# Kernel tuning notes

Hardware: AMD Instinct MI355X
Metric: run time of the kernel (lower is better)

The kernel has to match this reference:

```python
import jax, jax.numpy as jnp
import numpy as np

D_IN = 1024
D_OUT = 1024
NUM_HEADS = 16
HEAD_DIM = D_OUT // NUM_HEADS


def setup_inputs() -> dict:
    key = jax.random.key(0)
    k_x, k_qkv, k_pw, k_pb = jax.random.split(key, 4)
    x = jax.random.normal(k_x, (2, 2048, D_IN), dtype=jnp.float32)
    # torch nn.Linear(d_in, 3*d_out, bias=False): weight [3*d_out, d_in]
    w_qkv = jax.random.normal(k_qkv, (3 * D_OUT, D_IN), dtype=jnp.float32) * (1.0 / np.sqrt(D_IN))
    # proj: nn.Linear(d_out, d_out) with bias
    w_proj = jax.random.normal(k_pw, (D_OUT, D_OUT), dtype=jnp.float32) * (1.0 / np.sqrt(D_OUT))
    b_proj = jax.random.normal(k_pb, (D_OUT,), dtype=jnp.float32) * 0.01
    return {"x": x, "w_qkv": w_qkv, "w_proj": w_proj, "b_proj": b_proj}


def reference(x, w_qkv, w_proj, b_proj):
    B, S, _ = x.shape
    # fused QKV projection: [B,S,3*D_OUT]
    qkv = jnp.einsum('bsd,ed->bse', x, w_qkv)
    qkv = qkv.reshape(B, S, 3, NUM_HEADS, HEAD_DIM)
    q, k, v = jnp.moveaxis(qkv, 2, 0)  # each [B,S,H,Dh]
    scale = 1.0 / jnp.sqrt(jnp.asarray(HEAD_DIM, dtype=x.dtype))
    # scores [B,H,S,S]
    scores = jnp.einsum('bqhd,bkhd->bhqk', q, k) * scale
    causal = jnp.tril(jnp.ones((S, S), dtype=bool))
    scores = jnp.where(causal, scores, jnp.asarray(-jnp.inf, dtype=scores.dtype))
    attn = jax.nn.softmax(scores, axis=-1)
    ctx = jnp.einsum('bhqk,bkhd->bqhd', attn, v)  # [B,S,H,Dh]
    ctx = ctx.reshape(B, S, D_OUT)
    return jnp.einsum('bsd,ed->bse', ctx, w_proj) + b_proj
```

## Files before the change

kernel.cpp:

```cpp
#include <hip/hip_runtime.h>
#include <hip/hip_bf16.h>
#include <cstdint>

#define B_SZ   2
#define S_LEN  2048
#define NH     16
#define NT     32
#define LDA    72

using f32x4 = __attribute__((ext_vector_type(4))) float;
typedef __bf16 bf16x8 __attribute__((ext_vector_type(8)));
typedef __bf16 bf16x4 __attribute__((ext_vector_type(4)));

__device__ inline float bf2f(unsigned short u) {
    union { unsigned int i; float f; } v; v.i = ((unsigned int)u) << 16; return v.f;
}
__device__ inline unsigned short f2bf(float f) {
    union { float f; unsigned int i; } v; v.f = f;
    unsigned int r = v.i + 0x7fff + ((v.i >> 16) & 1);
    return (unsigned short)(r >> 16);
}
__device__ inline f32x4 mfma16(bf16x8 a, bf16x8 b, f32x4 c) {
    return __builtin_amdgcn_mfma_f32_16x16x32_bf16(a, b, c, 0, 0, 0);
}
__device__ inline void stC(float* C, size_t idx, float v)  { C[idx] = v; }
__device__ inline void stC(__bf16* C, size_t idx, float v) { ((unsigned short*)C)[idx] = f2bf(v); }

__global__ __launch_bounds__(256) void f2b2_kernel(
    const float* __restrict__ a, int na4, __bf16* __restrict__ outa,
    const float* __restrict__ b, int nb4, __bf16* __restrict__ outb)
{
    int i = blockIdx.x * blockDim.x + threadIdx.x;
    const float* src; __bf16* dst; int idx;
    if (i < na4)           { src = a; dst = outa; idx = i; }
    else if (i < na4 + nb4){ src = b; dst = outb; idx = i - na4; }
    else return;
    float4 v = ((const float4*)src)[idx];
    ushort4 o;
    o.x = f2bf(v.x); o.y = f2bf(v.y); o.z = f2bf(v.z); o.w = f2bf(v.w);
    ((ushort4*)dst)[idx] = o;
}

__global__ __launch_bounds__(256) void f2b_kernel(
    const float* __restrict__ in, __bf16* __restrict__ out, int n4)
{
    int i = blockIdx.x * blockDim.x + threadIdx.x;
    if (i < n4) {
        float4 v = ((const float4*)in)[i];
        ushort4 o;
        o.x = f2bf(v.x); o.y = f2bf(v.y); o.z = f2bf(v.z); o.w = f2bf(v.w);
        ((ushort4*)out)[i] = o;
    }
}

template <typename TO, int HAS_BIAS>
__global__ __launch_bounds__(256) void gemm128(
    const __bf16* __restrict__ A, const __bf16* __restrict__ W,
    const float* __restrict__ bias, TO* __restrict__ C,
    int M, int N, int K)
{
    __shared__ __bf16 Alds[2][128 * 32];
    __shared__ __bf16 Blds[2][128 * 32];
    const int tid  = threadIdx.x, lane = tid & 63, w = tid >> 6;
    const int c16  = lane & 15, quad = lane >> 4;
    const int mBase = blockIdx.y * 128, nBase = blockIdx.x * 128;
    const int moff = (w & 1) * 64, noff = (w >> 1) * 64;

    f32x4 acc[4][4];
#pragma unroll
    for (int i = 0; i < 4; ++i)
#pragma unroll
        for (int j = 0; j < 4; ++j) acc[i][j] = (f32x4){0.f, 0.f, 0.f, 0.f};

    auto stage = [&](int buf, int k0) {
#pragma unroll
        for (int p = 0; p < 2; ++p) {
            const int linear = p * 256 + tid;
            const int row = linear >> 2;
            const int seg = (linear & 3) ^ (row & 3);
            const int lbase = (p * 256 + w * 64) * 8;
            const __bf16* ga = A + (size_t)(mBase + row) * K + k0 + seg * 8;
            const __bf16* gb = W + (size_t)(nBase + row) * K + k0 + seg * 8;
            __builtin_amdgcn_global_load_lds(
                (const __attribute__((address_space(1))) void*)ga,
                (__attribute__((address_space(3))) void*)(&Alds[buf][lbase]), 16, 0, 0);
            __builtin_amdgcn_global_load_lds(
                (const __attribute__((address_space(1))) void*)gb,
                (__attribute__((address_space(3))) void*)(&Blds[buf][lbase]), 16, 0, 0);
        }
    };

    stage(0, 0);
    int cur = 0;
    for (int k0 = 0; k0 < K; k0 += 32) {
        __syncthreads();
        if (k0 + 32 < K) stage(cur ^ 1, k0 + 32);

        bf16x8 af[4], bw[4];
#pragma unroll
        for (int i = 0; i < 4; ++i) {
            const int rowA = moff + i * 16 + c16;
            af[i] = *(const bf16x8*)&Alds[cur][rowA * 32 + ((quad ^ (rowA & 3)) << 3)];
            const int rowB = noff + i * 16 + c16;
            bw[i] = *(const bf16x8*)&Blds[cur][rowB * 32 + ((quad ^ (rowB & 3)) << 3)];
        }
#pragma unroll
        for (int i = 0; i < 4; ++i)
#pragma unroll
            for (int j = 0; j < 4; ++j)
                acc[i][j] = mfma16(af[i], bw[j], acc[i][j]);
        cur ^= 1;
    }

#pragma unroll
    for (int j = 0; j < 4; ++j) {
        const int col = nBase + noff + j * 16 + c16;
        const float bv = HAS_BIAS ? bias[col] : 0.f;
#pragma unroll
        for (int i = 0; i < 4; ++i)
#pragma unroll
            for (int r = 0; r < 4; ++r) {
                const int row = mBase + moff + i * 16 + quad * 4 + r;
                stC(C, (size_t)row * N + col, acc[i][j][r] + bv);
            }
    }
}

template <typename TO, int HAS_BIAS>
__global__ __launch_bounds__(256) void gemm64(
    const __bf16* __restrict__ A, const __bf16* __restrict__ W,
    const float* __restrict__ bias, TO* __restrict__ C,
    int M, int N, int K)
{
    __shared__ __bf16 Alds[2][64 * 32];
    __shared__ __bf16 Blds[2][128 * 32];
    const int tid  = threadIdx.x, lane = tid & 63, w = tid >> 6;
    const int c16  = lane & 15, quad = lane >> 4;
    const int mBase = blockIdx.y * 64, nBase = blockIdx.x * 128;
    const int moff = (w & 1) * 32, noff = (w >> 1) * 64;

    f32x4 acc[2][4];
#pragma unroll
    for (int i = 0; i < 2; ++i)
#pragma unroll
        for (int j = 0; j < 4; ++j) acc[i][j] = (f32x4){0.f, 0.f, 0.f, 0.f};

    auto stage = [&](int buf, int k0) {
        {
            const int row = tid >> 2;
            const int seg = (tid & 3) ^ (row & 3);
            const int lbase = (w * 64) * 8;
            const __bf16* ga = A + (size_t)(mBase + row) * K + k0 + seg * 8;
            __builtin_amdgcn_global_load_lds(
                (const __attribute__((address_space(1))) void*)ga,
                (__attribute__((address_space(3))) void*)(&Alds[buf][lbase]), 16, 0, 0);
        }
#pragma unroll
        for (int p = 0; p < 2; ++p) {
            const int linear = p * 256 + tid;
            const int row = linear >> 2;
            const int seg = (linear & 3) ^ (row & 3);
            const int lbase = (p * 256 + w * 64) * 8;
            const __bf16* gb = W + (size_t)(nBase + row) * K + k0 + seg * 8;
            __builtin_amdgcn_global_load_lds(
                (const __attribute__((address_space(1))) void*)gb,
                (__attribute__((address_space(3))) void*)(&Blds[buf][lbase]), 16, 0, 0);
        }
    };

    stage(0, 0);
    int cur = 0;
    for (int k0 = 0; k0 < K; k0 += 32) {
        __syncthreads();
        if (k0 + 32 < K) stage(cur ^ 1, k0 + 32);

        bf16x8 af[2], bw[4];
#pragma unroll
        for (int i = 0; i < 2; ++i) {
            const int rowA = moff + i * 16 + c16;
            af[i] = *(const bf16x8*)&Alds[cur][rowA * 32 + ((quad ^ (rowA & 3)) << 3)];
        }
#pragma unroll
        for (int j = 0; j < 4; ++j) {
            const int rowB = noff + j * 16 + c16;
            bw[j] = *(const bf16x8*)&Blds[cur][rowB * 32 + ((quad ^ (rowB & 3)) << 3)];
        }
#pragma unroll
        for (int i = 0; i < 2; ++i)
#pragma unroll
            for (int j = 0; j < 4; ++j)
                acc[i][j] = mfma16(af[i], bw[j], acc[i][j]);
        cur ^= 1;
    }

#pragma unroll
    for (int j = 0; j < 4; ++j) {
        const int col = nBase + noff + j * 16 + c16;
        const float bv = HAS_BIAS ? bias[col] : 0.f;
#pragma unroll
        for (int i = 0; i < 2; ++i)
#pragma unroll
            for (int r = 0; r < 4; ++r) {
                const int row = mBase + moff + i * 16 + quad * 4 + r;
                stC(C, (size_t)row * N + col, acc[i][j][r] + bv);
            }
    }
}

__global__ __launch_bounds__(256) void attn(
    const __bf16* __restrict__ qkv, __bf16* __restrict__ ctx,
    float* __restrict__ opart, float* __restrict__ lpart)
{
    __shared__ __bf16 Qs[64 * LDA];
    __shared__ __bf16 Ks[64 * LDA];
    __shared__ __bf16 Vs[64 * LDA];
    __shared__ __bf16 Ps[64 * LDA];

    const int tid  = threadIdx.x;
    const int lane = tid & 63;
    const int w    = tid >> 6;
    const int c16  = lane & 15;
    const int quad = lane >> 4;
    const int bh = blockIdx.x, b = bh >> 4, h = bh & 15;
    const int y  = blockIdx.y;

    int qt, c0, c1, seg;
    bool split;
    if (y < 16)      { qt = 16 + y; const int half = (qt + 2) >> 1; c0 = 0;    c1 = half;   split = true;  seg = 0; }
    else if (y < 32) { qt = y;      const int half = (qt + 2) >> 1; c0 = half; c1 = qt + 1; split = true;  seg = 1; }
    else             { qt = 47 - y; c0 = 0; c1 = qt + 1; split = false; seg = 0; }
    const int qBase = qt * 64;
    const int segIdx = split ? ((bh * 16 + (qt - 16)) * 2 + seg) : 0;

    const float QS = 0.125f * 1.4426950408889634f;

    const int krow0 = tid >> 3;
    const int kd0   = (tid & 7) * 8;
    const int c16t = tid & 15;
    const int jh   = (tid >> 4) & 1;
    const int dblk = tid >> 5;

    const size_t rowB = (size_t)b * S_LEN;
    const __bf16* kp0 = qkv + (rowB + c0 * 64 + krow0) * 3072 + 1024 + h * 64 + kd0;
    const __bf16* kp1 = kp0 + (size_t)32 * 3072;
    const __bf16* vp0 = qkv + (rowB + c0 * 64 + 2 * jh * 16 + c16t) * 3072 + 2048 + h * 64 + dblk * 8;
    const __bf16* vp1 = vp0 + (size_t)16 * 3072;

    uint4 kr0 = *(const uint4*)kp0;
    uint4 kr1 = *(const uint4*)kp1;
    uint4 vr0 = *(const uint4*)vp0;
    uint4 vr1 = *(const uint4*)vp1;

#pragma unroll
    for (int p = 0; p < 2; ++p) {
        const int linear = p * 256 + tid;
        const int row = linear >> 3;
        const int d0 = (linear & 7) * 8;
        const __bf16* g = qkv + (rowB + qBase + row) * 3072 + h * 64 + d0;
        uint4 raw = *(const uint4*)g;
        const unsigned short* u = (const unsigned short*)&raw;
        unsigned short tmp[8];
#pragma unroll
        for (int jj = 0; jj < 8; ++jj) tmp[jj] = f2bf(bf2f(u[jj]) * QS);
        *(uint4*)&Qs[row * LDA + d0] = *(const uint4*)tmp;
    }
    __syncthreads();

    const bf16x8 aq0 = *(const bf16x8*)&Qs[(w * 16 + c16) * LDA + quad * 8];
    const bf16x8 aq1 = *(const bf16x8*)&Qs[(w * 16 + c16) * LDA + 32 + quad * 8];

    float l_r[4] = {0.f, 0.f, 0.f, 0.f};
    f32x4 acc_o[4];
#pragma unroll
    for (int j = 0; j < 4; ++j) acc_o[j] = (f32x4){0.f, 0.f, 0.f, 0.f};

    for (int cc = c0; cc < c1; ++cc) {
        *(uint4*)&Ks[krow0 * LDA + kd0]        = kr0;
        *(uint4*)&Ks[(krow0 + 32) * LDA + kd0] = kr1;
        {
            const unsigned short* e1 = (const unsigned short*)&vr0;
            const unsigned short* e2 = (const unsigned short*)&vr1;
#pragma unroll
            for (int d = 0; d < 8; ++d) {
                const unsigned pack = (unsigned)e1[d] | ((unsigned)e2[d] << 16);
                *(unsigned*)&Vs[(dblk * 8 + d) * LDA + c16t * 4 + 2 * jh] = pack;
            }
        }
        __syncthreads();

        if (cc + 1 < c1) {
            kp0 += (size_t)64 * 3072; kp1 += (size_t)64 * 3072;
            vp0 += (size_t)64 * 3072; vp1 += (size_t)64 * 3072;
            kr0 = *(const uint4*)kp0;
            kr1 = *(const uint4*)kp1;
            vr0 = *(const uint4*)vp0;
            vr1 = *(const uint4*)vp1;
        }

        f32x4 sc[4];
#pragma unroll
        for (int j = 0; j < 4; ++j) sc[j] = (f32x4){0.f, 0.f, 0.f, 0.f};
#pragma unroll
        for (int j = 0; j < 4; ++j) {
            bf16x8 bk0 = *(const bf16x8*)&Ks[(j * 16 + c16) * LDA + quad * 8];
            bf16x8 bk1 = *(const bf16x8*)&Ks[(j * 16 + c16) * LDA + 32 + quad * 8];
            sc[j] = mfma16(aq0, bk0, sc[j]);
            sc[j] = mfma16(aq1, bk1, sc[j]);
        }

        if (cc == qt) {
#pragma unroll
            for (int j = 0; j < 4; ++j) {
                const int key = cc * 64 + j * 16 + c16;
#pragma unroll
                for (int r = 0; r < 4; ++r) {
                    const int q = qBase + w * 16 + quad * 4 + r;
                    if (key > q) sc[j][r] = -1e30f;
                }
            }
        }

        float p_[4][4];
#pragma unroll
        for (int j = 0; j < 4; ++j)
#pragma unroll
            for (int r = 0; r < 4; ++r)
                p_[j][r] = exp2f(sc[j][r]);
#pragma unroll
        for (int r = 0; r < 4; ++r)
            l_r[r] += (p_[0][r] + p_[1][r]) + (p_[2][r] + p_[3][r]);

#pragma unroll
        for (int r = 0; r < 4; ++r) {
            bf16x4 pb;
            pb[0] = (__bf16)p_[0][r]; pb[1] = (__bf16)p_[1][r];
            pb[2] = (__bf16)p_[2][r]; pb[3] = (__bf16)p_[3][r];
            *(bf16x4*)&Ps[(w * 16 + quad * 4 + r) * LDA + c16 * 4] = pb;
        }

        bf16x8 ap0 = *(const bf16x8*)&Ps[(w * 16 + c16) * LDA + quad * 8];
        bf16x8 ap1 = *(const bf16x8*)&Ps[(w * 16 + c16) * LDA + 32 + quad * 8];
#pragma unroll
        for (int j = 0; j < 4; ++j) {
            bf16x8 bv0 = *(const bf16x8*)&Vs[(j * 16 + c16) * LDA + quad * 8];
            bf16x8 bv1 = *(const bf16x8*)&Vs[(j * 16 + c16) * LDA + 32 + quad * 8];
            acc_o[j] = mfma16(ap0, bv0, acc_o[j]);
            acc_o[j] = mfma16(ap1, bv1, acc_o[j]);
        }
        __syncthreads();
    }

    if (!split) {
#pragma unroll
        for (int r = 0; r < 4; ++r) {
            float l = l_r[r];
            l += __shfl_xor(l, 1);
            l += __shfl_xor(l, 2);
            l += __shfl_xor(l, 4);
            l += __shfl_xor(l, 8);
            const float inv = 1.0f / l;
            const size_t rowO = (rowB + qBase + w * 16 + quad * 4 + r) * 1024 + h * 64;
#pragma unroll
            for (int j = 0; j < 4; ++j)
                ctx[rowO + j * 16 + c16] = (__bf16)(acc_o[j][r] * inv);
        }
    } else {
        float* ob = opart + (size_t)segIdx * 4096;
#pragma unroll
        for (int r = 0; r < 4; ++r) {
            float l = l_r[r];
            l += __shfl_xor(l, 1);
            l += __shfl_xor(l, 2);
            l += __shfl_xor(l, 4);
            l += __shfl_xor(l, 8);
            const int qrow = w * 16 + quad * 4 + r;
            if (c16 == 0) lpart[segIdx * 64 + qrow] = l;
#pragma unroll
            for (int j = 0; j < 4; ++j)
                ob[qrow * 64 + j * 16 + c16] = acc_o[j][r];
        }
    }
}

__global__ __launch_bounds__(256) void attn_combine(
    const float* __restrict__ opart, const float* __restrict__ lpart,
    __bf16* __restrict__ ctx)
{
    const int blk = blockIdx.x;
    const int bh = blk >> 4, t = blk & 15;
    const int b = bh >> 4, h = bh & 15;
    const int qt = 16 + t;
    const int tid = threadIdx.x;
    const int q  = tid >> 2;
    const int d0 = (tid & 3) * 16;
    const int segA = blk * 2, segB = segA + 1;
    const float* oa = opart + (size_t)segA * 4096 + q * 64 + d0;
    const float* obp = opart + (size_t)segB * 4096 + q * 64 + d0;
    const float inv = 1.0f / (lpart[segA * 64 + q] + lpart[segB * 64 + q]);
    unsigned short outv[16];
#pragma unroll
    for (int i = 0; i < 4; ++i) {
        float4 a = ((const float4*)oa)[i];
        float4 c = ((const float4*)obp)[i];
        outv[4 * i + 0] = f2bf((a.x + c.x) * inv);
        outv[4 * i + 1] = f2bf((a.y + c.y) * inv);
        outv[4 * i + 2] = f2bf((a.z + c.z) * inv);
        outv[4 * i + 3] = f2bf((a.w + c.w) * inv);
    }
    __bf16* dst = ctx + ((size_t)(b * S_LEN + qt * 64 + q)) * 1024 + h * 64 + d0;
    *(uint4*)dst       = *(const uint4*)&outv[0];
    *(uint4*)(dst + 8) = *(const uint4*)&outv[8];
}

extern "C" void kernel_launch(void* const* d_in, const int* in_sizes, int n_in,
                              void* d_out, int out_size, void* d_ws, size_t ws_size,
                              hipStream_t stream) {
    const float* x      = (const float*)d_in[0];
    const float* w_qkv  = (const float*)d_in[1];
    const float* w_proj = (const float*)d_in[2];
    const float* b_proj = (const float*)d_in[3];
    float* out = (float*)d_out;

    __bf16* qkvb = (__bf16*)d_ws;
    __bf16* xb   = qkvb + (size_t)4096 * 3072;
    __bf16* wqb  = xb + (size_t)4096 * 1024;
    __bf16* ctxb = xb;
    __bf16* wpb  = wqb;
    float*  lpart = (float*)(wqb + (size_t)1024 * 1024);
    float* opart = out;

    const int M = B_SZ * S_LEN;
    const int nx4 = 4096 * 1024 / 4, nq4 = 3072 * 1024 / 4, np4 = 1024 * 1024 / 4;

    f2b2_kernel<<<(nx4 + nq4 + 255) / 256, 256, 0, stream>>>(x, nx4, xb, w_qkv, nq4, wqb);

    gemm128<__bf16, 0><<<dim3(3072 / 128, M / 128), 256, 0, stream>>>(
        xb, wqb, nullptr, qkvb, M, 3072, 1024);

    f2b_kernel<<<(np4 + 255) / 256, 256, 0, stream>>>(w_proj, wpb, np4);

    attn<<<dim3(B_SZ * NH, 48), 256, 0, stream>>>(qkvb, ctxb, opart, lpart);
    attn_combine<<<B_SZ * NH * 16, 256, 0, stream>>>(opart, lpart, ctxb);

    gemm64<float, 1><<<dim3(1024 / 128, M / 64), 256, 0, stream>>>(
        ctxb, wpb, b_proj, out, M, 1024, 1024);
}
```

Before: 184.9 us.

## Enlarge attention query tile to 128 rows with table-driven split scheduling

The attention kernel now processes 128 query rows per block (32 per wave) instead of 64, so each K/V tile loaded into shared memory feeds twice as many MFMAs. Work assignment moves to a constant lookup table that orders tiles largest-first and splits the eight longest query tiles into two key-range segments, with the combine kernel resized to match. This halves the number of blocks and K/V global reloads, at the cost of more registers and shared memory per block, fewer blocks in flight, and a coarser diagonal masking region.

```diff
diff --git a/kernel.cpp b/kernel.cpp
--- a/kernel.cpp
+++ b/kernel.cpp
@@ -5,7 +5,6 @@
 #define B_SZ   2
 #define S_LEN  2048
 #define NH     16
-#define NT     32
 #define LDA    72
 
 using f32x4 = __attribute__((ext_vector_type(4))) float;
@@ -25,6 +24,9 @@
 }
 __device__ inline void stC(float* C, size_t idx, float v)  { C[idx] = v; }
 __device__ inline void stC(__bf16* C, size_t idx, float v) { ((unsigned short*)C)[idx] = f2bf(v); }
+
+__constant__ unsigned char JT[24] = {15,15,7,14,14,13,13,6,12,12,11,11,5,10,10,9,9,4,8,8,3,2,1,0};
+__constant__ unsigned char JM[24] = { 0, 1,2, 0, 1, 0, 1,2, 0, 1, 0, 1,2, 0, 1,0,1,2,0,1,2,2,2,2};
 
 __global__ __launch_bounds__(256) void f2b2_kernel(
     const float* __restrict__ a, int na4, __bf16* __restrict__ outa,
@@ -211,10 +213,10 @@
     const __bf16* __restrict__ qkv, __bf16* __restrict__ ctx,
     float* __restrict__ opart, float* __restrict__ lpart)
 {
-    __shared__ __bf16 Qs[64 * LDA];
+    __shared__ __bf16 Qs[128 * LDA];
     __shared__ __bf16 Ks[64 * LDA];
     __shared__ __bf16 Vs[64 * LDA];
-    __shared__ __bf16 Ps[64 * LDA];
+    __shared__ __bf16 Ps[128 * LDA];
 
     const int tid  = threadIdx.x;
     const int lane = tid & 63;
@@ -224,13 +226,13 @@
     const int bh = blockIdx.x, b = bh >> 4, h = bh & 15;
     const int y  = blockIdx.y;
 
-    int qt, c0, c1, seg;
-    bool split;
-    if (y < 16)      { qt = 16 + y; const int half = (qt + 2) >> 1; c0 = 0;    c1 = half;   split = true;  seg = 0; }
-    else if (y < 32) { qt = y;      const int half = (qt + 2) >> 1; c0 = half; c1 = qt + 1; split = true;  seg = 1; }
-    else             { qt = 47 - y; c0 = 0; c1 = qt + 1; split = false; seg = 0; }
-    const int qBase = qt * 64;
-    const int segIdx = split ? ((bh * 16 + (qt - 16)) * 2 + seg) : 0;
+    const int t    = JT[y];
+    const int mode = JM[y];
+    const int qBase = t * 128;
+    const int c0 = (mode == 1) ? t + 1 : 0;
+    const int c1 = (mode == 0) ? t + 1 : 2 * t + 2;
+    const bool split = mode < 2;
+    const int segIdx = split ? ((bh * 8 + (t - 8)) * 2 + mode) : 0;
 
     const float QS = 0.125f * 1.4426950408889634f;
 
@@ -252,7 +254,7 @@
     uint4 vr1 = *(const uint4*)vp1;
 
 #pragma unroll
-    for (int p = 0; p < 2; ++p) {
+    for (int p = 0; p < 4; ++p) {
         const int linear = p * 256 + tid;
         const int row = linear >> 3;
         const int d0 = (linear & 7) * 8;
@@ -266,13 +268,19 @@
     }
     __syncthreads();
 
-    const bf16x8 aq0 = *(const bf16x8*)&Qs[(w * 16 + c16) * LDA + quad * 8];
-    const bf16x8 aq1 = *(const bf16x8*)&Qs[(w * 16 + c16) * LDA + 32 + quad * 8];
-
-    float l_r[4] = {0.f, 0.f, 0.f, 0.f};
-    f32x4 acc_o[4];
-#pragma unroll
-    for (int j = 0; j < 4; ++j) acc_o[j] = (f32x4){0.f, 0.f, 0.f, 0.f};
+    bf16x8 aq[2][2];
+#pragma unroll
+    for (int i = 0; i < 2; ++i) {
+        aq[i][0] = *(const bf16x8*)&Qs[(w * 32 + i * 16 + c16) * LDA + quad * 8];
+        aq[i][1] = *(const bf16x8*)&Qs[(w * 32 + i * 16 + c16) * LDA + 32 + quad * 8];
+    }
+
+    float l_r[2][4] = {};
+    f32x4 acc_o[2][4];
+#pragma unroll
+    for (int i = 0; i < 2; ++i)
+#pragma unroll
+        for (int j = 0; j < 4; ++j) acc_o[i][j] = (f32x4){0.f, 0.f, 0.f, 0.f};
 
     for (int cc = c0; cc < c1; ++cc) {
         *(uint4*)&Ks[krow0 * LDA + kd0]        = kr0;
@@ -297,89 +305,94 @@
             vr1 = *(const uint4*)vp1;
         }
 
-        f32x4 sc[4];
-#pragma unroll
-        for (int j = 0; j < 4; ++j) sc[j] = (f32x4){0.f, 0.f, 0.f, 0.f};
+        f32x4 sc[2][4];
+#pragma unroll
+        for (int i = 0; i < 2; ++i)
+#pragma unroll
+            for (int j = 0; j < 4; ++j) sc[i][j] = (f32x4){0.f, 0.f, 0.f, 0.f};
 #pragma unroll
         for (int j = 0; j < 4; ++j) {
             bf16x8 bk0 = *(const bf16x8*)&Ks[(j * 16 + c16) * LDA + quad * 8];
             bf16x8 bk1 = *(const bf16x8*)&Ks[(j * 16 + c16) * LDA + 32 + quad * 8];
-            sc[j] = mfma16(aq0, bk0, sc[j]);
-            sc[j] = mfma16(aq1, bk1, sc[j]);
-        }
-
-        if (cc == qt) {
-#pragma unroll
-            for (int j = 0; j < 4; ++j) {
-                const int key = cc * 64 + j * 16 + c16;
-#pragma unroll
-                for (int r = 0; r < 4; ++r) {
-                    const int q = qBase + w * 16 + quad * 4 + r;
-                    if (key > q) sc[j][r] = -1e30f;
+#pragma unroll
+            for (int i = 0; i < 2; ++i) {
+                sc[i][j] = mfma16(aq[i][0], bk0, sc[i][j]);
+                sc[i][j] = mfma16(aq[i][1], bk1, sc[i][j]);
+            }
+        }
+
+        if (cc >= 2 * t) {
+#pragma unroll
+            for (int i = 0; i < 2; ++i)
+#pragma unroll
+                for (int j = 0; j < 4; ++j) {
+                    const int key = cc * 64 + j * 16 + c16;
+#pragma unroll
+                    for (int r = 0; r < 4; ++r) {
+                        const int q = qBase + w * 32 + i * 16 + quad * 4 + r;
+                        if (key > q) sc[i][j][r] = -1e30f;
+                    }
                 }
-            }
-        }
-
-        float p_[4][4];
-#pragma unroll
-        for (int j = 0; j < 4; ++j)
-#pragma unroll
-            for (int r = 0; r < 4; ++r)
-                p_[j][r] = exp2f(sc[j][r]);
-#pragma unroll
-        for (int r = 0; r < 4; ++r)
-            l_r[r] += (p_[0][r] + p_[1][r]) + (p_[2][r] + p_[3][r]);
-
-#pragma unroll
-        for (int r = 0; r < 4; ++r) {
-            bf16x4 pb;
-            pb[0] = (__bf16)p_[0][r]; pb[1] = (__bf16)p_[1][r];
-            pb[2] = (__bf16)p_[2][r]; pb[3] = (__bf16)p_[3][r];
-            *(bf16x4*)&Ps[(w * 16 + quad * 4 + r) * LDA + c16 * 4] = pb;
-        }
-
-        bf16x8 ap0 = *(const bf16x8*)&Ps[(w * 16 + c16) * LDA + quad * 8];
-        bf16x8 ap1 = *(const bf16x8*)&Ps[(w * 16 + c16) * LDA + 32 + quad * 8];
+        }
+
+#pragma unroll
+        for (int i = 0; i < 2; ++i)
+#pragma unroll
+            for (int r = 0; r < 4; ++r) {
+                const float e0 = exp2f(sc[i][0][r]);
+                const float e1 = exp2f(sc[i][1][r]);
+                const float e2 = exp2f(sc[i][2][r]);
+                const float e3 = exp2f(sc[i][3][r]);
+                l_r[i][r] += (e0 + e1) + (e2 + e3);
+                bf16x4 pb;
+                pb[0] = (__bf16)e0; pb[1] = (__bf16)e1;
+                pb[2] = (__bf16)e2; pb[3] = (__bf16)e3;
+                *(bf16x4*)&Ps[(w * 32 + i * 16 + quad * 4 + r) * LDA + c16 * 4] = pb;
+            }
+
+        bf16x8 ap[2][2];
+#pragma unroll
+        for (int i = 0; i < 2; ++i) {
+            ap[i][0] = *(const bf16x8*)&Ps[(w * 32 + i * 16 + c16) * LDA + quad * 8];
+            ap[i][1] = *(const bf16x8*)&Ps[(w * 32 + i * 16 + c16) * LDA + 32 + quad * 8];
+        }
 #pragma unroll
         for (int j = 0; j < 4; ++j) {
             bf16x8 bv0 = *(const bf16x8*)&Vs[(j * 16 + c16) * LDA + quad * 8];
             bf16x8 bv1 = *(const bf16x8*)&Vs[(j * 16 + c16) * LDA + 32 + quad * 8];
-            acc_o[j] = mfma16(ap0, bv0, acc_o[j]);
-            acc_o[j] = mfma16(ap1, bv1, acc_o[j]);
+#pragma unroll
+            for (int i = 0; i < 2; ++i) {
+                acc_o[i][j] = mfma16(ap[i][0], bv0, acc_o[i][j]);
+                acc_o[i][j] = mfma16(ap[i][1], bv1, acc_o[i][j]);
+            }
         }
         __syncthreads();
     }
 
-    if (!split) {
+#pragma unroll
+    for (int i = 0; i < 2; ++i)
 #pragma unroll
         for (int r = 0; r < 4; ++r) {
-            float l = l_r[r];
+            float l = l_r[i][r];
             l += __shfl_xor(l, 1);
             l += __shfl_xor(l, 2);
             l += __shfl_xor(l, 4);
             l += __shfl_xor(l, 8);
-            const float inv = 1.0f / l;
-            const size_t rowO = (rowB + qBase + w * 16 + quad * 4 + r) * 1024 + h * 64;
-#pragma unroll
-            for (int j = 0; j < 4; ++j)
-                ctx[rowO + j * 16 + c16] = (__bf16)(acc_o[j][r] * inv);
-        }
-    } else {
-        float* ob = opart + (size_t)segIdx * 4096;
-#pragma unroll
-        for (int r = 0; r < 4; ++r) {
-            float l = l_r[r];
-            l += __shfl_xor(l, 1);
-            l += __shfl_xor(l, 2);
-            l += __shfl_xor(l, 4);
-            l += __shfl_xor(l, 8);
-            const int qrow = w * 16 + quad * 4 + r;
-            if (c16 == 0) lpart[segIdx * 64 + qrow] = l;
-#pragma unroll
-            for (int j = 0; j < 4; ++j)
-                ob[qrow * 64 + j * 16 + c16] = acc_o[j][r];
-        }
-    }
+            const int qrow = w * 32 + i * 16 + quad * 4 + r;
+            if (!split) {
+                const float inv = 1.0f / l;
+                const size_t rowO = (rowB + qBase + qrow) * 1024 + h * 64;
+#pragma unroll
+                for (int j = 0; j < 4; ++j)
+                    ctx[rowO + j * 16 + c16] = (__bf16)(acc_o[i][j][r] * inv);
+            } else {
+                float* ob = opart + (size_t)segIdx * 8192;
+                if (c16 == 0) lpart[segIdx * 128 + qrow] = l;
+#pragma unroll
+                for (int j = 0; j < 4; ++j)
+                    ob[qrow * 64 + j * 16 + c16] = acc_o[i][j][r];
+            }
+        }
 }
 
 __global__ __launch_bounds__(256) void attn_combine(
@@ -387,19 +400,18 @@
     __bf16* __restrict__ ctx)
 {
     const int blk = blockIdx.x;
-    const int bh = blk >> 4, t = blk & 15;
+    const int bh = blk >> 3, t = 8 + (blk & 7);
     const int b = bh >> 4, h = bh & 15;
-    const int qt = 16 + t;
     const int tid = threadIdx.x;
-    const int q  = tid >> 2;
-    const int d0 = (tid & 3) * 16;
+    const int q  = tid >> 1;
+    const int d0 = (tid & 1) * 32;
     const int segA = blk * 2, segB = segA + 1;
-    const float* oa = opart + (size_t)segA * 4096 + q * 64 + d0;
-    const float* obp = opart + (size_t)segB * 4096 + q * 64 + d0;
-    const float inv = 1.0f / (lpart[segA * 64 + q] + lpart[segB * 64 + q]);
-    unsigned short outv[16];
-#pragma unroll
-    for (int i = 0; i < 4; ++i) {
+    const float* oa  = opart + (size_t)segA * 8192 + q * 64 + d0;
+    const float* obp = opart + (size_t)segB * 8192 + q * 64 + d0;
+    const float inv = 1.0f / (lpart[segA * 128 + q] + lpart[segB * 128 + q]);
+    unsigned short outv[32];
+#pragma unroll
+    for (int i = 0; i < 8; ++i) {
         float4 a = ((const float4*)oa)[i];
         float4 c = ((const float4*)obp)[i];
         outv[4 * i + 0] = f2bf((a.x + c.x) * inv);
@@ -407,9 +419,10 @@
         outv[4 * i + 2] = f2bf((a.z + c.z) * inv);
         outv[4 * i + 3] = f2bf((a.w + c.w) * inv);
     }
-    __bf16* dst = ctx + ((size_t)(b * S_LEN + qt * 64 + q)) * 1024 + h * 64 + d0;
-    *(uint4*)dst       = *(const uint4*)&outv[0];
-    *(uint4*)(dst + 8) = *(const uint4*)&outv[8];
+    __bf16* dst = ctx + ((size_t)(b * S_LEN + t * 128 + q)) * 1024 + h * 64 + d0;
+#pragma unroll
+    for (int i = 0; i < 4; ++i)
+        *(uint4*)(dst + i * 8) = *(const uint4*)&outv[8 * i];
 }
 
 extern "C" void kernel_launch(void* const* d_in, const int* in_sizes, int n_in,
@@ -439,8 +452,8 @@
 
     f2b_kernel<<<(np4 + 255) / 256, 256, 0, stream>>>(w_proj, wpb, np4);
 
-    attn<<<dim3(B_SZ * NH, 48), 256, 0, stream>>>(qkvb, ctxb, opart, lpart);
-    attn_combine<<<B_SZ * NH * 16, 256, 0, stream>>>(opart, lpart, ctxb);
+    attn<<<dim3(B_SZ * NH, 24), 256, 0, stream>>>(qkvb, ctxb, opart, lpart);
+    attn_combine<<<B_SZ * NH * 8, 256, 0, stream>>>(opart, lpart, ctxb);
 
     gemm64<float, 1><<<dim3(1024 / 128, M / 64), 256, 0, stream>>>(
         ctxb, wpb, b_proj, out, M, 1024, 1024);
```

Measured after the change: 193.3 us. 1.05x slower.
